# Optimization experiments

Hardware: AMD Instinct MI355X
Metric: run time of the kernel (lower is better)

Reference implementation:

```python
import jax, jax.numpy as jnp
import numpy as np

D_MODEL = 1024
N_HEADS = 16
HEAD_DIM = D_MODEL // N_HEADS


def setup_inputs() -> dict:
    key = jax.random.key(0)
    k1, k2, k3 = jax.random.split(key, 3)
    scale = 1.0 / np.sqrt(D_MODEL)
    x = jax.random.normal(k1, (4, 2048, D_MODEL), dtype=jnp.float32)
    w_qkv = jax.random.normal(k2, (D_MODEL, 3 * D_MODEL), dtype=jnp.float32) * scale
    b_qkv = jnp.zeros((3 * D_MODEL,), dtype=jnp.float32)
    w_proj = jax.random.normal(k3, (D_MODEL, D_MODEL), dtype=jnp.float32) * scale
    b_proj = jnp.zeros((D_MODEL,), dtype=jnp.float32)
    return {"x": x, "w_qkv": w_qkv, "b_qkv": b_qkv, "w_proj": w_proj, "b_proj": b_proj}


def reference(x, w_qkv, b_qkv, w_proj, b_proj):
    B, T, C = x.shape
    H, Dh = N_HEADS, HEAD_DIM
    qkv = x @ w_qkv + b_qkv                       # (B, T, 3C)
    qkv = qkv.reshape(B, T, 3, H, Dh)
    q = qkv[:, :, 0].transpose(0, 2, 1, 3)        # (B, H, T, Dh)
    k = qkv[:, :, 1].transpose(0, 2, 1, 3)
    v = qkv[:, :, 2].transpose(0, 2, 1, 3)
    att = jnp.einsum('bhqd,bhkd->bhqk', q, k) / jnp.sqrt(jnp.float32(Dh))
    causal = jnp.tril(jnp.ones((T, T), dtype=bool))
    att = jnp.where(causal[None, None], att, -jnp.inf)
    att = jax.nn.softmax(att, axis=-1)
    y = jnp.einsum('bhqk,bhkd->bhqd', att, v)     # (B, H, T, Dh)
    y = y.transpose(0, 2, 1, 3).reshape(B, T, C)
    return y @ w_proj + b_proj
```

## Files before the change

### kernel.cpp

```cpp
#include <hip/hip_runtime.h>
#include <hip/hip_bf16.h>
#include <math.h>

typedef __bf16 bf16_t;
typedef __bf16 bf16x4 __attribute__((ext_vector_type(4)));
typedef __bf16 bf16x8 __attribute__((ext_vector_type(8)));
typedef float floatx4 __attribute__((ext_vector_type(4)));
typedef unsigned int u32;

#define AS1 __attribute__((address_space(1)))
#define AS3 __attribute__((address_space(3)))

__device__ bf16_t g_xb[8192 * 1024];
__device__ bf16_t g_wqkvT[3072 * 1024];
__device__ bf16_t g_wprojT[1024 * 1024];
__device__ float  g_bqkv[3072];
__device__ float  g_bproj[1024];
__device__ bf16_t g_qkv[3ull * 64 * 2048 * 64];
#define HBREG (64ull * 2048 * 64)

__global__ __launch_bounds__(256) void cvt_x(const float* __restrict__ src,
                                             const float* __restrict__ bq,
                                             const float* __restrict__ bp) {
  int blk = blockIdx.x;
  int tid = threadIdx.x;
  if (blk < 4096) {
    int i0 = (blk * 256 + tid) * 8;
    const float4* s = (const float4*)src;
    float4 a = s[i0 / 4], b = s[i0 / 4 + 1];
    bf16x8 v;
    v[0] = (bf16_t)a.x; v[1] = (bf16_t)a.y; v[2] = (bf16_t)a.z; v[3] = (bf16_t)a.w;
    v[4] = (bf16_t)b.x; v[5] = (bf16_t)b.y; v[6] = (bf16_t)b.z; v[7] = (bf16_t)b.w;
    *(bf16x8*)&g_xb[i0] = v;
  } else if (blk == 4096) {
    for (int i = tid; i < 3072; i += 256) g_bqkv[i] = bq[i];
  } else {
    for (int i = tid; i < 1024; i += 256) g_bproj[i] = bp[i];
  }
}

__global__ __launch_bounds__(256) void tr64(const float* __restrict__ wqkv,
                                            const float* __restrict__ wproj) {
  __shared__ bf16_t tile[64][65];
  const int R = 1024;
  int bx = blockIdx.x;
  const float* in;
  bf16_t* out;
  int C, c0;
  if (bx < 48) { in = wqkv; out = g_wqkvT; C = 3072; c0 = bx * 64; }
  else         { in = wproj; out = g_wprojT; C = 1024; c0 = (bx - 48) * 64; }
  int r0 = blockIdx.y * 64;
  int tid = threadIdx.x;
#pragma unroll
  for (int it = 0; it < 16; ++it) {
    int idx = tid + it * 256;
    int r = idx >> 6, c = idx & 63;
    tile[r][c] = (bf16_t)in[(size_t)(r0 + r) * C + (c0 + c)];
  }
  __syncthreads();
#pragma unroll
  for (int it = 0; it < 16; ++it) {
    int idx = tid + it * 256;
    int r = idx >> 6, c = idx & 63;
    out[(size_t)(c0 + r) * R + (r0 + c)] = tile[c][r];
  }
}

#define MFMA16(a, b, c) __builtin_amdgcn_mfma_f32_16x16x32_bf16(a, b, c, 0, 0, 0)
#define SB0() __builtin_amdgcn_sched_barrier(0)
#define PH_MID()                                          \
  do {                                                    \
    SB0();                                                \
    __builtin_amdgcn_s_barrier();                         \
    SB0();                                                \
    asm volatile("s_waitcnt lgkmcnt(0)" ::: "memory");    \
    SB0();                                                \
  } while (0)
#define PH_END()                                          \
  do {                                                    \
    SB0();                                                \
    __builtin_amdgcn_s_barrier();                         \
    SB0();                                                \
  } while (0)

__global__ __launch_bounds__(512) void gemm256(float* __restrict__ out_ext,
                                               int M, int N, int K,
                                               int amode, int bsel, int cmode) {
  __shared__ alignas(16) bf16_t As[2][256 * 64];
  __shared__ alignas(16) bf16_t Bs[2][256 * 64];
  (void)M;
  const bf16_t* Ag = (amode == 0) ? g_xb : g_qkv;
  const bf16_t* Bt = bsel ? g_wprojT : g_wqkvT;
  const float* bias = bsel ? g_bproj : g_bqkv;
  const int tid = threadIdx.x;

  int gx = gridDim.x;
  int nwg = gx * gridDim.y;
  int lin = blockIdx.y * gx + blockIdx.x;
  int swz = (lin & 7) * (nwg >> 3) + (lin >> 3);
  int bx = swz % gx, by = swz / gx;
  const int m0 = by * 256, n0 = bx * 256;

  const int lane = tid & 63, wave = tid >> 6;
  const int wm = wave >> 2, wn = wave & 3;
  const int quad = lane >> 4, l16 = lane & 15;

  const u32 xv = (u32)(l16 & 7) << 4;
  const u32 sq0 = ((u32)quad * 16u) ^ xv;
  const u32 sq1 = (64u + (u32)quad * 16u) ^ xv;
  const u32 a_rb = (u32)(wm * 64 + l16) * 128u;
  const u32 b_rb = (u32)(wn * 32 + l16) * 128u;

  u32 row_j[2], scol_j[2];
#pragma unroll
  for (int j = 0; j < 2; ++j) {
    u32 L = ((u32)j * 512u + (u32)tid) * 16u;
    u32 y = L ^ (((L >> 7) & 7u) << 4);
    row_j[j] = y >> 7;
    scol_j[j] = (y & 127u) >> 1;
  }
  u32 a_go[2][2], b_go[2][2], akts;
  if (amode == 0) {
#pragma unroll
    for (int h = 0; h < 2; ++h)
#pragma unroll
      for (int j = 0; j < 2; ++j)
        a_go[h][j] = (u32)(m0 + h * 128 + (int)row_j[j]) * (u32)K + scol_j[j];
    akts = 64u;
  } else {
#pragma unroll
    for (int h = 0; h < 2; ++h)
#pragma unroll
      for (int j = 0; j < 2; ++j) {
        int m = m0 + h * 128 + (int)row_j[j];
        a_go[h][j] = (u32)(m >> 11) * 2097152u + (u32)(m & 2047) * 64u + scol_j[j];
      }
    akts = 131072u;
  }
#pragma unroll
  for (int h = 0; h < 2; ++h)
#pragma unroll
    for (int j = 0; j < 2; ++j)
      b_go[h][j] = (u32)(n0 + h * 128 + (int)row_j[j]) * (u32)K + scol_j[j];

  auto stageA = [&](int kt_, int h_) {
#pragma unroll
    for (int j = 0; j < 2; ++j)
      __builtin_amdgcn_global_load_lds(
          (const AS1 void*)(Ag + (size_t)(a_go[h_][j] + (u32)kt_ * akts)),
          (AS3 void*)&As[kt_ & 1][h_ * 8192 + (j * 512 + tid) * 8], 16, 0, 0);
  };
  auto stageB = [&](int kt_, int h_) {
#pragma unroll
    for (int j = 0; j < 2; ++j)
      __builtin_amdgcn_global_load_lds(
          (const AS1 void*)(Bt + (size_t)(b_go[h_][j] + (u32)kt_ * 64u)),
          (AS3 void*)&Bs[kt_ & 1][h_ * 8192 + (j * 512 + tid) * 8], 16, 0, 0);
  };

  floatx4 acc[2][4][2][2] = {};
  const int NT = K >> 6;

  stageA(0, 0); SB0(); stageB(0, 0); SB0();
  stageA(0, 1); SB0(); stageB(0, 1); SB0();
  asm volatile("s_waitcnt vmcnt(4)" ::: "memory");
  __builtin_amdgcn_s_barrier();
  SB0();

  for (int kt = 0; kt < NT; ++kt) {
    const int b = kt & 1;
    const char* Ab = (const char*)&As[b][0];
    const char* Bb = (const char*)&Bs[b][0];
    bf16x8 af[4][2], bv[2][2], bw[2][2];

#pragma unroll
    for (int mf = 0; mf < 4; ++mf) {
      af[mf][0] = *(const bf16x8*)(Ab + (a_rb + mf * 2048 + sq0));
      af[mf][1] = *(const bf16x8*)(Ab + (a_rb + mf * 2048 + sq1));
    }
#pragma unroll
    for (int nf = 0; nf < 2; ++nf) {
      bv[nf][0] = *(const bf16x8*)(Bb + (b_rb + nf * 2048 + sq0));
      bv[nf][1] = *(const bf16x8*)(Bb + (b_rb + nf * 2048 + sq1));
    }
    if (kt + 1 < NT) stageA(kt + 1, 0);
    PH_MID();
    __builtin_amdgcn_s_setprio(1);
#pragma unroll
    for (int mf = 0; mf < 4; ++mf)
#pragma unroll
      for (int nf = 0; nf < 2; ++nf) {
        acc[0][mf][0][nf] = MFMA16(af[mf][0], bv[nf][0], acc[0][mf][0][nf]);
        acc[0][mf][0][nf] = MFMA16(af[mf][1], bv[nf][1], acc[0][mf][0][nf]);
      }
    __builtin_amdgcn_s_setprio(0);
    SB0();
    if (kt + 1 < NT) asm volatile("s_waitcnt vmcnt(2)" ::: "memory");
    else             asm volatile("s_waitcnt vmcnt(0)" ::: "memory");
    __builtin_amdgcn_s_barrier();
    SB0();

#pragma unroll
    for (int nf = 0; nf < 2; ++nf) {
      bw[nf][0] = *(const bf16x8*)(Bb + (b_rb + 16384 + nf * 2048 + sq0));
      bw[nf][1] = *(const bf16x8*)(Bb + (b_rb + 16384 + nf * 2048 + sq1));
    }
    if (kt + 1 < NT) stageB(kt + 1, 0);
    PH_MID();
    __builtin_amdgcn_s_setprio(1);
#pragma unroll
    for (int mf = 0; mf < 4; ++mf)
#pragma unroll
      for (int nf = 0; nf < 2; ++nf) {
        acc[0][mf][1][nf] = MFMA16(af[mf][0], bw[nf][0], acc[0][mf][1][nf]);
        acc[0][mf][1][nf] = MFMA16(af[mf][1], bw[nf][1], acc[0][mf][1][nf]);
      }
    __builtin_amdgcn_s_setprio(0);
    PH_END();

#pragma unroll
    for (int mf = 0; mf < 4; ++mf) {
      af[mf][0] = *(const bf16x8*)(Ab + (a_rb + 16384 + mf * 2048 + sq0));
      af[mf][1] = *(const bf16x8*)(Ab + (a_rb + 16384 + mf * 2048 + sq1));
    }
    if (kt + 1 < NT) stageA(kt + 1, 1);
    PH_MID();
    __builtin_amdgcn_s_setprio(1);
#pragma unroll
    for (int mf = 0; mf < 4; ++mf)
#pragma unroll
      for (int nf = 0; nf < 2; ++nf) {
        acc[1][mf][1][nf] = MFMA16(af[mf][0], bw[nf][0], acc[1][mf][1][nf]);
        acc[1][mf][1][nf] = MFMA16(af[mf][1], bw[nf][1], acc[1][mf][1][nf]);
      }
    __builtin_amdgcn_s_setprio(0);
    PH_END();

#pragma unroll
    for (int nf = 0; nf < 2; ++nf) {
      bv[nf][0] = *(const bf16x8*)(Bb + (b_rb + nf * 2048 + sq0));
      bv[nf][1] = *(const bf16x8*)(Bb + (b_rb + nf * 2048 + sq1));
    }
    if (kt + 1 < NT) stageB(kt + 1, 1);
    PH_MID();
    __builtin_amdgcn_s_setprio(1);
#pragma unroll
    for (int mf = 0; mf < 4; ++mf)
#pragma unroll
      for (int nf = 0; nf < 2; ++nf) {
        acc[1][mf][0][nf] = MFMA16(af[mf][0], bv[nf][0], acc[1][mf][0][nf]);
        acc[1][mf][0][nf] = MFMA16(af[mf][1], bv[nf][1], acc[1][mf][0][nf]);
      }
    __builtin_amdgcn_s_setprio(0);
    SB0();
    if (kt + 1 < NT) asm volatile("s_waitcnt vmcnt(4)" ::: "memory");
    else             asm volatile("s_waitcnt vmcnt(0)" ::: "memory");
    __builtin_amdgcn_s_barrier();
    SB0();
  }

#pragma unroll
  for (int mh = 0; mh < 2; ++mh)
#pragma unroll
  for (int mf = 0; mf < 4; ++mf)
#pragma unroll
  for (int nh = 0; nh < 2; ++nh)
#pragma unroll
  for (int nf = 0; nf < 2; ++nf) {
    int ncol = n0 + wn * 32 + nh * 128 + nf * 16 + l16;
    float bb = bias[ncol];
    int mbase = m0 + wm * 64 + mh * 128 + mf * 16 + quad * 4;
    if (cmode == 0) {
      int which = ncol >> 10;
      int h = (ncol >> 6) & 15;
      int d = ncol & 63;
      int b_ = mbase >> 11, t = mbase & 2047;
      if (which == 2) {
        bf16x4 pk;
#pragma unroll
        for (int r = 0; r < 4; ++r) pk[r] = (bf16_t)(acc[mh][mf][nh][nf][r] + bb);
        size_t dst = 2 * HBREG + ((size_t)((b_ * 16 + h) * 64 + d)) * 2048 + t;
        *(bf16x4*)&g_qkv[dst] = pk;
      } else {
        size_t base = (size_t)which * HBREG +
                      ((size_t)((b_ * 16 + h) * 2048 + t)) * 64 + d;
#pragma unroll
        for (int r = 0; r < 4; ++r)
          g_qkv[base + (size_t)r * 64] = (bf16_t)(acc[mh][mf][nh][nf][r] + bb);
      }
    } else {
#pragma unroll
      for (int r = 0; r < 4; ++r)
        out_ext[(size_t)(mbase + r) * N + ncol] = acc[mh][mf][nh][nf][r] + bb;
    }
  }
}

__global__ __launch_bounds__(256) void attn64() {
  const int LDW = 72;
  __shared__ bf16_t Qs[64 * 72];
  __shared__ bf16_t Ks[64 * 72];
  __shared__ bf16_t Vt[64 * 72];
  bf16_t* Ps = Qs;
  const float C1 = 0.1803368801111204f;
  const float C2 = -23.083120654223414f;
  const int tid = threadIdx.x;
  const int qpair = blockIdx.y;
  const int bh = blockIdx.x;
  const bf16_t* Qb  = g_qkv + (size_t)bh * 2048 * 64;
  const bf16_t* Kb  = g_qkv + HBREG + (size_t)bh * 2048 * 64;
  const bf16_t* VTb = g_qkv + 2 * HBREG + (size_t)bh * 64 * 2048;
  bf16_t* Yb = g_qkv + (size_t)bh * 2048 * 64;
  const int lane = tid & 63, wave = tid >> 6;
  const int quad = lane >> 4, l16 = lane & 15;
  const int row0 = tid >> 3, c80 = (tid & 7) * 8;

  bf16x8 ones8;
#pragma unroll
  for (int j = 0; j < 8; ++j) ones8[j] = (bf16_t)1.0f;

  for (int ph = 0; ph < 2; ++ph) {
    const int qi = ph ? (31 - qpair) : qpair;
    const int q0 = qi * 64;

    *(bf16x8*)&Qs[row0 * LDW + c80] =
        *(const bf16x8*)&Qb[(size_t)(q0 + row0) * 64 + c80];
    *(bf16x8*)&Qs[(row0 + 32) * LDW + c80] =
        *(const bf16x8*)&Qb[(size_t)(q0 + row0 + 32) * 64 + c80];
    __syncthreads();
    bf16x8 aq0 = *(const bf16x8*)&Qs[(wave * 16 + l16) * LDW + quad * 8];
    bf16x8 aq1 = *(const bf16x8*)&Qs[(wave * 16 + l16) * LDW + 32 + quad * 8];

    floatx4 o[4] = {};
    floatx4 osum = {};

    bf16x8 kp0 = *(const bf16x8*)&Kb[(size_t)row0 * 64 + c80];
    bf16x8 kp1 = *(const bf16x8*)&Kb[(size_t)(row0 + 32) * 64 + c80];
    bf16x8 vp0 = *(const bf16x8*)&VTb[(size_t)row0 * 2048 + c80];
    bf16x8 vp1 = *(const bf16x8*)&VTb[(size_t)(row0 + 32) * 2048 + c80];

    const int ntiles = qi + 1;
    for (int kt = 0; kt < ntiles; ++kt) {
      __syncthreads();
      *(bf16x8*)&Ks[row0 * LDW + c80] = kp0;
      *(bf16x8*)&Ks[(row0 + 32) * LDW + c80] = kp1;
      *(bf16x8*)&Vt[row0 * LDW + c80] = vp0;
      *(bf16x8*)&Vt[(row0 + 32) * LDW + c80] = vp1;
      if (kt + 1 < ntiles) {
        const int k1 = (kt + 1) * 64;
        kp0 = *(const bf16x8*)&Kb[(size_t)(k1 + row0) * 64 + c80];
        kp1 = *(const bf16x8*)&Kb[(size_t)(k1 + row0 + 32) * 64 + c80];
        vp0 = *(const bf16x8*)&VTb[(size_t)row0 * 2048 + k1 + c80];
        vp1 = *(const bf16x8*)&VTb[(size_t)(row0 + 32) * 2048 + k1 + c80];
      }
      __syncthreads();

      const int k0 = kt * 64;
      floatx4 s[4];
      __builtin_amdgcn_s_setprio(1);
#pragma unroll
      for (int tn = 0; tn < 4; ++tn) {
        bf16x8 bk0 = *(const bf16x8*)&Ks[(tn * 16 + l16) * LDW + quad * 8];
        bf16x8 bk1 = *(const bf16x8*)&Ks[(tn * 16 + l16) * LDW + 32 + quad * 8];
        floatx4 z = {};
        z = __builtin_amdgcn_mfma_f32_16x16x32_bf16(aq0, bk0, z, 0, 0, 0);
        z = __builtin_amdgcn_mfma_f32_16x16x32_bf16(aq1, bk1, z, 0, 0, 0);
        s[tn] = z;
      }
      __builtin_amdgcn_s_setprio(0);

      if (kt == qi) {
#pragma unroll
        for (int tn = 0; tn < 4; ++tn) {
          int kcol = k0 + tn * 16 + l16;
#pragma unroll
          for (int r = 0; r < 4; ++r) {
            int qrow = q0 + wave * 16 + quad * 4 + r;
            float p = exp2f(fminf(fmaf(s[tn][r], C1, C2), 30.f));
            s[tn][r] = (kcol > qrow) ? 0.f : p;
          }
        }
      } else {
#pragma unroll
        for (int tn = 0; tn < 4; ++tn)
#pragma unroll
          for (int r = 0; r < 4; ++r)
            s[tn][r] = exp2f(fminf(fmaf(s[tn][r], C1, C2), 30.f));
      }

      bf16_t* Pw = &Ps[wave * 16 * LDW];
#pragma unroll
      for (int tn = 0; tn < 4; ++tn)
#pragma unroll
        for (int r = 0; r < 4; ++r)
          Pw[(quad * 4 + r) * LDW + tn * 16 + l16] = (bf16_t)s[tn][r];

      bf16x8 ap0 = *(const bf16x8*)&Pw[l16 * LDW + quad * 8];
      bf16x8 ap1 = *(const bf16x8*)&Pw[l16 * LDW + 32 + quad * 8];
      __builtin_amdgcn_s_setprio(1);
#pragma unroll
      for (int tn = 0; tn < 4; ++tn) {
        bf16x8 bv0 = *(const bf16x8*)&Vt[(tn * 16 + l16) * LDW + quad * 8];
        bf16x8 bv1 = *(const bf16x8*)&Vt[(tn * 16 + l16) * LDW + 32 + quad * 8];
        o[tn] = __builtin_amdgcn_mfma_f32_16x16x32_bf16(ap0, bv0, o[tn], 0, 0, 0);
        o[tn] = __builtin_amdgcn_mfma_f32_16x16x32_bf16(ap1, bv1, o[tn], 0, 0, 0);
      }
      osum = __builtin_amdgcn_mfma_f32_16x16x32_bf16(ap0, ones8, osum, 0, 0, 0);
      osum = __builtin_amdgcn_mfma_f32_16x16x32_bf16(ap1, ones8, osum, 0, 0, 0);
      __builtin_amdgcn_s_setprio(0);
    }

#pragma unroll
    for (int r = 0; r < 4; ++r) {
      float inv = 1.0f / osum[r];
      int t = q0 + wave * 16 + quad * 4 + r;
#pragma unroll
      for (int tn = 0; tn < 4; ++tn) {
        int d = tn * 16 + l16;
        Yb[(size_t)t * 64 + d] = (bf16_t)(o[tn][r] * inv);
      }
    }
    __syncthreads();
  }
}

extern "C" void kernel_launch(void* const* d_in, const int* in_sizes, int n_in,
                              void* d_out, int out_size, void* d_ws, size_t ws_size,
                              hipStream_t stream) {
  const float* x      = (const float*)d_in[0];
  const float* w_qkv  = (const float*)d_in[1];
  const float* b_qkv  = (const float*)d_in[2];
  const float* w_proj = (const float*)d_in[3];
  const float* b_proj = (const float*)d_in[4];
  (void)d_ws; (void)ws_size;

  cvt_x<<<4098, 256, 0, stream>>>(x, b_qkv, b_proj);
  tr64<<<dim3(64, 16), 256, 0, stream>>>(w_qkv, w_proj);

  gemm256<<<dim3(12, 32), 512, 0, stream>>>(nullptr, 8192, 3072, 1024, 0, 0, 0);

  attn64<<<dim3(64, 16), 256, 0, stream>>>();

  gemm256<<<dim3(4, 32), 512, 0, stream>>>((float*)d_out, 8192, 1024, 1024, 1, 1, 1);
}
```

Before: 304.9 us.

## Double-buffer K/V tiles and transpose MFMA operands in causal attention kernel

```diff
diff --git a/kernel.cpp b/kernel.cpp
--- a/kernel.cpp
+++ b/kernel.cpp
@@ -298,10 +298,9 @@
 
 __global__ __launch_bounds__(256) void attn64() {
   const int LDW = 72;
-  __shared__ bf16_t Qs[64 * 72];
-  __shared__ bf16_t Ks[64 * 72];
-  __shared__ bf16_t Vt[64 * 72];
-  bf16_t* Ps = Qs;
+  __shared__ bf16_t Ks[2][64 * 72];
+  __shared__ bf16_t Vt[2][64 * 72];
+  __shared__ bf16_t Ps[4 * 16 * 72];
   const float C1 = 0.1803368801111204f;
   const float C2 = -23.083120654223414f;
   const int tid = threadIdx.x;
@@ -314,6 +313,7 @@
   const int lane = tid & 63, wave = tid >> 6;
   const int quad = lane >> 4, l16 = lane & 15;
   const int row0 = tid >> 3, c80 = (tid & 7) * 8;
+  bf16_t* Pw = &Ps[wave * 16 * LDW];
 
   bf16x8 ones8;
 #pragma unroll
@@ -322,14 +322,10 @@
   for (int ph = 0; ph < 2; ++ph) {
     const int qi = ph ? (31 - qpair) : qpair;
     const int q0 = qi * 64;
-
-    *(bf16x8*)&Qs[row0 * LDW + c80] =
-        *(const bf16x8*)&Qb[(size_t)(q0 + row0) * 64 + c80];
-    *(bf16x8*)&Qs[(row0 + 32) * LDW + c80] =
-        *(const bf16x8*)&Qb[(size_t)(q0 + row0 + 32) * 64 + c80];
-    __syncthreads();
-    bf16x8 aq0 = *(const bf16x8*)&Qs[(wave * 16 + l16) * LDW + quad * 8];
-    bf16x8 aq1 = *(const bf16x8*)&Qs[(wave * 16 + l16) * LDW + 32 + quad * 8];
+    const int qrow = q0 + wave * 16 + l16;
+
+    bf16x8 aq0 = *(const bf16x8*)&Qb[(size_t)qrow * 64 + quad * 8];
+    bf16x8 aq1 = *(const bf16x8*)&Qb[(size_t)qrow * 64 + 32 + quad * 8];
 
     floatx4 o[4] = {};
     floatx4 osum = {};
@@ -340,12 +336,14 @@
     bf16x8 vp1 = *(const bf16x8*)&VTb[(size_t)(row0 + 32) * 2048 + c80];
 
     const int ntiles = qi + 1;
+    int c = 0;
+    __syncthreads();
+
     for (int kt = 0; kt < ntiles; ++kt) {
-      __syncthreads();
-      *(bf16x8*)&Ks[row0 * LDW + c80] = kp0;
-      *(bf16x8*)&Ks[(row0 + 32) * LDW + c80] = kp1;
-      *(bf16x8*)&Vt[row0 * LDW + c80] = vp0;
-      *(bf16x8*)&Vt[(row0 + 32) * LDW + c80] = vp1;
+      *(bf16x8*)&Ks[c][row0 * LDW + c80] = kp0;
+      *(bf16x8*)&Ks[c][(row0 + 32) * LDW + c80] = kp1;
+      *(bf16x8*)&Vt[c][row0 * LDW + c80] = vp0;
+      *(bf16x8*)&Vt[c][(row0 + 32) * LDW + c80] = vp1;
       if (kt + 1 < ntiles) {
         const int k1 = (kt + 1) * 64;
         kp0 = *(const bf16x8*)&Kb[(size_t)(k1 + row0) * 64 + c80];
@@ -360,26 +358,24 @@
       __builtin_amdgcn_s_setprio(1);
 #pragma unroll
       for (int tn = 0; tn < 4; ++tn) {
-        bf16x8 bk0 = *(const bf16x8*)&Ks[(tn * 16 + l16) * LDW + quad * 8];
-        bf16x8 bk1 = *(const bf16x8*)&Ks[(tn * 16 + l16) * LDW + 32 + quad * 8];
+        bf16x8 bk0 = *(const bf16x8*)&Ks[c][(tn * 16 + l16) * LDW + quad * 8];
+        bf16x8 bk1 = *(const bf16x8*)&Ks[c][(tn * 16 + l16) * LDW + 32 + quad * 8];
         floatx4 z = {};
-        z = __builtin_amdgcn_mfma_f32_16x16x32_bf16(aq0, bk0, z, 0, 0, 0);
-        z = __builtin_amdgcn_mfma_f32_16x16x32_bf16(aq1, bk1, z, 0, 0, 0);
+        z = __builtin_amdgcn_mfma_f32_16x16x32_bf16(bk0, aq0, z, 0, 0, 0);
+        z = __builtin_amdgcn_mfma_f32_16x16x32_bf16(bk1, aq1, z, 0, 0, 0);
         s[tn] = z;
       }
       __builtin_amdgcn_s_setprio(0);
 
       if (kt == qi) {
 #pragma unroll
-        for (int tn = 0; tn < 4; ++tn) {
-          int kcol = k0 + tn * 16 + l16;
+        for (int tn = 0; tn < 4; ++tn)
 #pragma unroll
           for (int r = 0; r < 4; ++r) {
-            int qrow = q0 + wave * 16 + quad * 4 + r;
+            int kcol = k0 + tn * 16 + quad * 4 + r;
             float p = exp2f(fminf(fmaf(s[tn][r], C1, C2), 30.f));
             s[tn][r] = (kcol > qrow) ? 0.f : p;
           }
-        }
       } else {
 #pragma unroll
         for (int tn = 0; tn < 4; ++tn)
@@ -388,39 +384,38 @@
             s[tn][r] = exp2f(fminf(fmaf(s[tn][r], C1, C2), 30.f));
       }
 
-      bf16_t* Pw = &Ps[wave * 16 * LDW];
-#pragma unroll
-      for (int tn = 0; tn < 4; ++tn)
-#pragma unroll
-        for (int r = 0; r < 4; ++r)
-          Pw[(quad * 4 + r) * LDW + tn * 16 + l16] = (bf16_t)s[tn][r];
-
-      bf16x8 ap0 = *(const bf16x8*)&Pw[l16 * LDW + quad * 8];
-      bf16x8 ap1 = *(const bf16x8*)&Pw[l16 * LDW + 32 + quad * 8];
+#pragma unroll
+      for (int tn = 0; tn < 4; ++tn) {
+        bf16x4 pk;
+#pragma unroll
+        for (int r = 0; r < 4; ++r) pk[r] = (bf16_t)s[tn][r];
+        *(bf16x4*)&Pw[l16 * LDW + tn * 16 + quad * 4] = pk;
+      }
+      bf16x8 pp0 = *(const bf16x8*)&Pw[l16 * LDW + quad * 8];
+      bf16x8 pp1 = *(const bf16x8*)&Pw[l16 * LDW + 32 + quad * 8];
+
       __builtin_amdgcn_s_setprio(1);
 #pragma unroll
       for (int tn = 0; tn < 4; ++tn) {
-        bf16x8 bv0 = *(const bf16x8*)&Vt[(tn * 16 + l16) * LDW + quad * 8];
-        bf16x8 bv1 = *(const bf16x8*)&Vt[(tn * 16 + l16) * LDW + 32 + quad * 8];
-        o[tn] = __builtin_amdgcn_mfma_f32_16x16x32_bf16(ap0, bv0, o[tn], 0, 0, 0);
-        o[tn] = __builtin_amdgcn_mfma_f32_16x16x32_bf16(ap1, bv1, o[tn], 0, 0, 0);
-      }
-      osum = __builtin_amdgcn_mfma_f32_16x16x32_bf16(ap0, ones8, osum, 0, 0, 0);
-      osum = __builtin_amdgcn_mfma_f32_16x16x32_bf16(ap1, ones8, osum, 0, 0, 0);
+        bf16x8 av0 = *(const bf16x8*)&Vt[c][(tn * 16 + l16) * LDW + quad * 8];
+        bf16x8 av1 = *(const bf16x8*)&Vt[c][(tn * 16 + l16) * LDW + 32 + quad * 8];
+        o[tn] = __builtin_amdgcn_mfma_f32_16x16x32_bf16(av0, pp0, o[tn], 0, 0, 0);
+        o[tn] = __builtin_amdgcn_mfma_f32_16x16x32_bf16(av1, pp1, o[tn], 0, 0, 0);
+      }
+      osum = __builtin_amdgcn_mfma_f32_16x16x32_bf16(ones8, pp0, osum, 0, 0, 0);
+      osum = __builtin_amdgcn_mfma_f32_16x16x32_bf16(ones8, pp1, osum, 0, 0, 0);
       __builtin_amdgcn_s_setprio(0);
-    }
-
-#pragma unroll
-    for (int r = 0; r < 4; ++r) {
-      float inv = 1.0f / osum[r];
-      int t = q0 + wave * 16 + quad * 4 + r;
-#pragma unroll
-      for (int tn = 0; tn < 4; ++tn) {
-        int d = tn * 16 + l16;
-        Yb[(size_t)t * 64 + d] = (bf16_t)(o[tn][r] * inv);
-      }
-    }
-    __syncthreads();
+      c ^= 1;
+    }
+
+    float inv = 1.0f / osum[0];
+#pragma unroll
+    for (int tn = 0; tn < 4; ++tn) {
+      bf16x4 yv;
+#pragma unroll
+      for (int r = 0; r < 4; ++r) yv[r] = (bf16_t)(o[tn][r] * inv);
+      *(bf16x4*)&Yb[(size_t)qrow * 64 + tn * 16 + quad * 4] = yv;
+    }
   }
 }
 
```

Result: faster. 296.8 us (-2.7%).
